# Kernel optimization log

Measured on AMD Instinct MI355X. Metric: run time of the kernel, lower is better.

## Reference

```python
import jax, jax.numpy as jnp
import numpy as np
from jax import lax

IN_FEATURES = 8192
OUT_FEATURES = 28672


def _unpack3(qweight, infeatures):
    """Unpack GPTQ-style 3-bit weights.

    qweight: (infeatures//32*3, O) int32. Every 3 consecutive int32 rows hold
    32 packed 3-bit values per column (GPTQ quant.py packing): values 0-9 in
    word0 bits [0..30), value 10 split over word0[30:32]|word1[0:1],
    values 11-20 in word1 bits [1..31), value 21 split over word1[31:32]|word2[0:2],
    values 22-31 in word2 bits [2..32).
    Returns float32 (infeatures, O) with raw quant codes in [0, 8).
    """
    O = qweight.shape[1]
    G = infeatures // 32
    q = lax.bitcast_convert_type(qweight, jnp.uint32).reshape(G, 3, O)
    w0, w1, w2 = q[:, 0], q[:, 1], q[:, 2]
    sh = jnp.arange(10, dtype=jnp.uint32)  # 10 whole values per word
    v0 = (w0[:, None, :] >> (3 * sh)[None, :, None]) & 7          # (G,10,O)
    v10 = (((w0 >> 30) & 3) | ((w1 & 1) << 2))[:, None, :]        # (G,1,O)
    v1 = (w1[:, None, :] >> (3 * sh + 1)[None, :, None]) & 7       # (G,10,O)
    v21 = (((w1 >> 31) & 1) | ((w2 & 3) << 1))[:, None, :]        # (G,1,O)
    v2 = (w2[:, None, :] >> (3 * sh + 2)[None, :, None]) & 7       # (G,10,O)
    vals = jnp.concatenate([v0, v10, v1, v21, v2], axis=1)        # (G,32,O)
    return vals.reshape(infeatures, O).astype(jnp.float32)


def setup_inputs() -> dict:
    key = jax.random.key(0)
    k1, k2, k3, k4, k5 = jax.random.split(key, 5)
    x = jax.random.normal(k1, (1, IN_FEATURES), dtype=jnp.float32)
    qweight = jax.random.randint(k2, (IN_FEATURES // 32 * 3, OUT_FEATURES), 0, 2147483647, dtype=jnp.int32)
    scales = jax.random.uniform(k3, (OUT_FEATURES, 1), dtype=jnp.float32)
    zeros = jax.random.normal(k4, (OUT_FEATURES, 1), dtype=jnp.float32)
    bias = jax.random.normal(k5, (OUT_FEATURES,), dtype=jnp.float32)
    return {"x": x, "qweight": qweight, "scales": scales, "zeros": zeros, "bias": bias}


def reference(x, qweight, scales, zeros, bias):
    infeatures = x.shape[-1]
    q = _unpack3(qweight, infeatures)            # (K, O) float codes
    # per-output-channel dequant: W[k, o] = scales[o] * q[k, o] - zeros[o]
    W = scales.T * q - zeros.T                   # (K, O)
    y = x @ W + bias                             # (1, O)
    return y
```

## Files before the change

### kernel.cpp

```cpp
#include <hip/hip_runtime.h>
#include <stdint.h>


constexpr int O_FEAT  = 28672;
constexpr int IN_FEAT = 8192;
constexpr int NGROUP  = IN_FEAT / 32;
constexpr int SPLIT   = 8;
constexpr int GPB     = NGROUP / SPLIT;

__global__ __launch_bounds__(256) void q3_init(const float* __restrict__ x,
                                               const float* __restrict__ zeros,
                                               const float* __restrict__ bias,
                                               float* __restrict__ out) {
  float s = 0.f;
  const float4* x4 = reinterpret_cast<const float4*>(x);
  for (int i = threadIdx.x; i < IN_FEAT / 4; i += 256) {
    float4 t = x4[i];
    s += (t.x + t.y) + (t.z + t.w);
  }
  #pragma unroll
  for (int off = 32; off > 0; off >>= 1) s += __shfl_down(s, off, 64);
  __shared__ float ls[4];
  if ((threadIdx.x & 63) == 0) ls[threadIdx.x >> 6] = s;
  __syncthreads();
  float S = (ls[0] + ls[1]) + (ls[2] + ls[3]);
  int o = blockIdx.x * 256 + threadIdx.x;
  out[o] = bias[o] - zeros[o] * S;
}

__global__ __launch_bounds__(256) void q3_gemv(const float* __restrict__ x,
                                               const uint32_t* __restrict__ qw,
                                               const float* __restrict__ scales,
                                               float* __restrict__ out) {
  const int o  = blockIdx.x * 256 + threadIdx.x;
  const int g0 = blockIdx.y * GPB;
  float acc0 = 0.f, acc1 = 0.f, acc2 = 0.f;
  const uint32_t* qp = qw + (size_t)(3 * g0) * O_FEAT + o;
  const float*    xp = x + g0 * 32;

  for (int g = 0; g < GPB; ++g) {
    uint32_t w0 = qp[0];
    uint32_t w1 = qp[O_FEAT];
    uint32_t w2 = qp[2 * O_FEAT];
    qp += 3 * O_FEAT;

    float xv[32];
    const float4* x4 = reinterpret_cast<const float4*>(xp);
    #pragma unroll
    for (int u = 0; u < 8; ++u) {
      float4 t = x4[u];
      xv[4 * u + 0] = t.x; xv[4 * u + 1] = t.y;
      xv[4 * u + 2] = t.z; xv[4 * u + 3] = t.w;
    }
    xp += 32;

    #pragma unroll
    for (int j = 0; j < 10; ++j)
      acc0 += xv[j] * (float)((w0 >> (3 * j)) & 7u);
    acc0 += xv[10] * (float)((w0 >> 30) | ((w1 & 1u) << 2));
    #pragma unroll
    for (int j = 0; j < 10; ++j)
      acc1 += xv[11 + j] * (float)((w1 >> (3 * j + 1)) & 7u);
    acc1 += xv[21] * (float)((w1 >> 31) | ((w2 & 3u) << 1));
    #pragma unroll
    for (int j = 0; j < 10; ++j)
      acc2 += xv[22 + j] * (float)((w2 >> (3 * j + 2)) & 7u);
  }

  atomicAdd(&out[o], scales[o] * ((acc0 + acc1) + acc2));
}

extern "C" void kernel_launch(void* const* d_in, const int* in_sizes, int n_in,
                              void* d_out, int out_size, void* d_ws, size_t ws_size,
                              hipStream_t stream) {
  const float*    x      = (const float*)d_in[0];
  const uint32_t* qw     = (const uint32_t*)d_in[1];
  const float*    scales = (const float*)d_in[2];
  const float*    zeros  = (const float*)d_in[3];
  const float*    bias   = (const float*)d_in[4];
  float*          out    = (float*)d_out;

  q3_init<<<dim3(O_FEAT / 256), dim3(256), 0, stream>>>(x, zeros, bias, out);
  q3_gemv<<<dim3(O_FEAT / 256, SPLIT), dim3(256), 0, stream>>>(x, qw, scales, out);
}
```

Measured before the change: 150.0 us.

## Vectorize weight loads to uint4 and replace atomics with workspace split-K reduction

Each thread now handles four adjacent output columns and reads the packed weights with 128-bit uint4 loads. The K split goes from 8 to 32 so the grid keeps enough blocks. Partial sums are written to a workspace instead of being added atomically to the output, and a finish kernel sums the 32 partials and applies scale, zero-point and bias. This targets weight-load efficiency and atomic contention, at the cost of extra workspace traffic (32 x O floats) and more registers per thread.

After: 143.5 us. 1.05x faster.

```diff
diff --git a/kernel.cpp b/kernel.cpp
--- a/kernel.cpp
+++ b/kernel.cpp
@@ -5,13 +5,65 @@
 constexpr int O_FEAT  = 28672;
 constexpr int IN_FEAT = 8192;
 constexpr int NGROUP  = IN_FEAT / 32;
-constexpr int SPLIT   = 8;
+constexpr int SPLIT   = 32;
 constexpr int GPB     = NGROUP / SPLIT;
+constexpr int O4      = O_FEAT / 4;
 
-__global__ __launch_bounds__(256) void q3_init(const float* __restrict__ x,
-                                               const float* __restrict__ zeros,
-                                               const float* __restrict__ bias,
-                                               float* __restrict__ out) {
+__device__ __forceinline__ void dot_group(uint32_t w0, uint32_t w1, uint32_t w2,
+                                          const float xv[32], float& acc) {
+  float a0 = acc, a1 = 0.f, a2 = 0.f;
+  #pragma unroll
+  for (int j = 0; j < 10; ++j) a0 += xv[j] * (float)((w0 >> (3 * j)) & 7u);
+  a0 += xv[10] * (float)((w0 >> 30) | ((w1 & 1u) << 2));
+  #pragma unroll
+  for (int j = 0; j < 10; ++j) a1 += xv[11 + j] * (float)((w1 >> (3 * j + 1)) & 7u);
+  a1 += xv[21] * (float)((w1 >> 31) | ((w2 & 3u) << 1));
+  #pragma unroll
+  for (int j = 0; j < 10; ++j) a2 += xv[22 + j] * (float)((w2 >> (3 * j + 2)) & 7u);
+  acc = a0 + (a1 + a2);
+}
+
+__global__ __launch_bounds__(256) void q3_partial(const float* __restrict__ x,
+                                                  const uint4* __restrict__ qw4,
+                                                  float* __restrict__ part) {
+  const int tcol4 = blockIdx.x * 256 + threadIdx.x;
+  const int g0    = blockIdx.y * GPB;
+  const uint4* qp = qw4 + (size_t)(3 * g0) * O4 + tcol4;
+  const float* xp = x + g0 * 32;
+  float acc0 = 0.f, acc1 = 0.f, acc2 = 0.f, acc3 = 0.f;
+
+  for (int g = 0; g < GPB; ++g) {
+    uint4 wa = qp[0];
+    uint4 wb = qp[O4];
+    uint4 wc = qp[2 * O4];
+    qp += 3 * O4;
+
+    float xv[32];
+    const float4* x4 = reinterpret_cast<const float4*>(xp);
+    #pragma unroll
+    for (int u = 0; u < 8; ++u) {
+      float4 t = x4[u];
+      xv[4 * u + 0] = t.x; xv[4 * u + 1] = t.y;
+      xv[4 * u + 2] = t.z; xv[4 * u + 3] = t.w;
+    }
+    xp += 32;
+
+    dot_group(wa.x, wb.x, wc.x, xv, acc0);
+    dot_group(wa.y, wb.y, wc.y, xv, acc1);
+    dot_group(wa.z, wb.z, wc.z, xv, acc2);
+    dot_group(wa.w, wb.w, wc.w, xv, acc3);
+  }
+
+  float4 r = make_float4(acc0, acc1, acc2, acc3);
+  reinterpret_cast<float4*>(part)[(size_t)blockIdx.y * O4 + tcol4] = r;
+}
+
+__global__ __launch_bounds__(256) void q3_finish(const float* __restrict__ x,
+                                                 const float* __restrict__ part,
+                                                 const float* __restrict__ scales,
+                                                 const float* __restrict__ zeros,
+                                                 const float* __restrict__ bias,
+                                                 float* __restrict__ out) {
   float s = 0.f;
   const float4* x4 = reinterpret_cast<const float4*>(x);
   for (int i = threadIdx.x; i < IN_FEAT / 4; i += 256) {
@@ -24,62 +76,25 @@
   if ((threadIdx.x & 63) == 0) ls[threadIdx.x >> 6] = s;
   __syncthreads();
   float S = (ls[0] + ls[1]) + (ls[2] + ls[3]);
+
   int o = blockIdx.x * 256 + threadIdx.x;
-  out[o] = bias[o] - zeros[o] * S;
-}
-
-__global__ __launch_bounds__(256) void q3_gemv(const float* __restrict__ x,
-                                               const uint32_t* __restrict__ qw,
-                                               const float* __restrict__ scales,
-                                               float* __restrict__ out) {
-  const int o  = blockIdx.x * 256 + threadIdx.x;
-  const int g0 = blockIdx.y * GPB;
-  float acc0 = 0.f, acc1 = 0.f, acc2 = 0.f;
-  const uint32_t* qp = qw + (size_t)(3 * g0) * O_FEAT + o;
-  const float*    xp = x + g0 * 32;
-
-  for (int g = 0; g < GPB; ++g) {
-    uint32_t w0 = qp[0];
-    uint32_t w1 = qp[O_FEAT];
-    uint32_t w2 = qp[2 * O_FEAT];
-    qp += 3 * O_FEAT;
-
-    float xv[32];
-    const float4* x4 = reinterpret_cast<const float4*>(xp);
-    #pragma unroll
-    for (int u = 0; u < 8; ++u) {
-      float4 t = x4[u];
-      xv[4 * u + 0] = t.x; xv[4 * u + 1] = t.y;
-      xv[4 * u + 2] = t.z; xv[4 * u + 3] = t.w;
-    }
-    xp += 32;
-
-    #pragma unroll
-    for (int j = 0; j < 10; ++j)
-      acc0 += xv[j] * (float)((w0 >> (3 * j)) & 7u);
-    acc0 += xv[10] * (float)((w0 >> 30) | ((w1 & 1u) << 2));
-    #pragma unroll
-    for (int j = 0; j < 10; ++j)
-      acc1 += xv[11 + j] * (float)((w1 >> (3 * j + 1)) & 7u);
-    acc1 += xv[21] * (float)((w1 >> 31) | ((w2 & 3u) << 1));
-    #pragma unroll
-    for (int j = 0; j < 10; ++j)
-      acc2 += xv[22 + j] * (float)((w2 >> (3 * j + 2)) & 7u);
-  }
-
-  atomicAdd(&out[o], scales[o] * ((acc0 + acc1) + acc2));
+  float sum = 0.f;
+  #pragma unroll
+  for (int y = 0; y < SPLIT; ++y) sum += part[(size_t)y * O_FEAT + o];
+  out[o] = scales[o] * sum - zeros[o] * S + bias[o];
 }
 
 extern "C" void kernel_launch(void* const* d_in, const int* in_sizes, int n_in,
                               void* d_out, int out_size, void* d_ws, size_t ws_size,
                               hipStream_t stream) {
-  const float*    x      = (const float*)d_in[0];
-  const uint32_t* qw     = (const uint32_t*)d_in[1];
-  const float*    scales = (const float*)d_in[2];
-  const float*    zeros  = (const float*)d_in[3];
-  const float*    bias   = (const float*)d_in[4];
-  float*          out    = (float*)d_out;
+  const float* x      = (const float*)d_in[0];
+  const uint4* qw4    = (const uint4*)d_in[1];
+  const float* scales = (const float*)d_in[2];
+  const float* zeros  = (const float*)d_in[3];
+  const float* bias   = (const float*)d_in[4];
+  float*       out    = (float*)d_out;
+  float*       part   = (float*)d_ws;
 
-  q3_init<<<dim3(O_FEAT / 256), dim3(256), 0, stream>>>(x, zeros, bias, out);
-  q3_gemv<<<dim3(O_FEAT / 256, SPLIT), dim3(256), 0, stream>>>(x, qw, scales, out);
+  q3_partial<<<dim3(O_FEAT / (256 * 4), SPLIT), dim3(256), 0, stream>>>(x, qw4, part);
+  q3_finish<<<dim3(O_FEAT / 256), dim3(256), 0, stream>>>(x, part, scales, zeros, bias, out);
 }
```
